# Kernel optimization log

Measured on AMD Instinct MI355X. Metric: run time of the kernel, lower is better.

The kernel has to match this reference:

```python
import jax, jax.numpy as jnp
import numpy as np

TOP_K = 3
K3, S3, P3 = 3, 1, 1  # unfold_kernel_size, stride, padding (lv3)


def unfold(x, k, stride, pad):
    """torch.nn.functional.unfold: [N,C,H,W] -> [N, C*k*k, L]."""
    patches = jax.lax.conv_general_dilated_patches(
        x, (k, k), (stride, stride), [(pad, pad), (pad, pad)],
        dimension_numbers=('NCHW', 'OIHW', 'NCHW'))  # [N, C*k*k, gh, gw]
    n, d, gh, gw = patches.shape
    return patches.reshape(n, d, gh * gw)


def fold(cols, H, W, k, stride, pad):
    """torch.nn.functional.fold (col2im, overlap-add): [N,C*k*k,L] -> [N,C,H,W]."""
    n, d, L = cols.shape
    C = d // (k * k)
    gh = (H + 2 * pad - k) // stride + 1
    gw = (W + 2 * pad - k) // stride + 1
    cols = cols.reshape(n, C, k, k, gh, gw)
    out = jnp.zeros((n, C, H + 2 * pad, W + 2 * pad), cols.dtype)
    for i in range(k):
        for j in range(k):
            out = out.at[:, :, i:i + stride * gh:stride,
                         j:j + stride * gw:stride].add(cols[:, :, i, j])
    return out[:, :, pad:pad + H, pad:pad + W]


def _l2norm(x, axis):
    # F.normalize: x / max(||x||_2, 1e-12)
    return x / jnp.maximum(jnp.sqrt(jnp.sum(x * x, axis=axis, keepdims=True)), 1e-12)


def search_transfer(lr_lv3, refsr_lv3, ref_lv1, ref_lv2, ref_lv3):
    n, _, h, w = lr_lv3.shape
    k2, s2, p2 = 2 * K3, 2 * S3, 2 * P3
    k1, s1, p1 = 4 * K3, 4 * S3, 4 * P3

    # --- SearchPatches (original passes padding=stride, stride=padding; equal here) ---
    Q = unfold(lr_lv3, K3, P3, S3)            # [N, D, Lq]
    Kc = unfold(refsr_lv3, K3, P3, S3)        # [N, D, Lr]
    Kn = _l2norm(jnp.swapaxes(Kc, 1, 2), 2)   # [N, Lr, D]
    Qn = _l2norm(Q, 1)                        # [N, D, Lq]
    R = jnp.einsum('nrd,ndq->nrq', Kn, Qn)    # cosine sims [N, Lr, Lq]
    vals, idx = jax.lax.top_k(jnp.swapaxes(R, 1, 2), TOP_K)  # [N, Lq, K]
    soft = jnp.swapaxes(vals, 1, 2)           # [N, K, Lq]
    hard = jnp.swapaxes(idx, 1, 2)            # [N, K, Lq]

    # --- Transfer: unfold ref textures (padding=stride per original code) ---
    V3 = unfold(ref_lv3, K3, S3, S3)          # [N, 256*9,  Lq]
    V2 = unfold(ref_lv2, k2, s2, s2)          # [N, 128*36, Lq]
    V1 = unfold(ref_lv1, k1, s1, s1)          # [N, 64*144, Lq]

    # overlap divisors are constant across top-k iterations -> compute once
    div3 = fold(jnp.ones_like(V3), h, w, K3, S3, S3)
    div2 = fold(jnp.ones_like(V2), 2 * h, 2 * w, k2, s2, s2)
    div1 = fold(jnp.ones_like(V1), 4 * h, 4 * w, k1, s1, s1)

    Sl, T3l, T2l, T1l = [], [], [], []
    for i in range(TOP_K):
        hi = hard[:, i, :][:, None, :]        # [N, 1, Lq], broadcasts over feature dim
        g3 = jnp.take_along_axis(V3, hi, axis=2)
        g2 = jnp.take_along_axis(V2, hi, axis=2)
        g1 = jnp.take_along_axis(V1, hi, axis=2)
        T3l.append(fold(g3, h, w, K3, S3, S3) / div3)
        T2l.append(fold(g2, 2 * h, 2 * w, k2, s2, s2) / div2)
        T1l.append(fold(g1, 4 * h, 4 * w, k1, s1, s1) / div1)
        Sl.append(soft[:, i, :].reshape(n, 1, h // S3, w // S3))
    return (jnp.stack(Sl), jnp.stack(T3l), jnp.stack(T2l), jnp.stack(T1l))


def setup_inputs() -> dict:
    key = jax.random.key(0)
    ks = jax.random.split(key, 5)
    return {
        'lr_lv3':    jax.random.normal(ks[0], (2, 256, 48, 48),   dtype=jnp.float32),
        'refsr_lv3': jax.random.normal(ks[1], (2, 256, 48, 48),   dtype=jnp.float32),
        'ref_lv1':   jax.random.normal(ks[2], (2, 64, 192, 192),  dtype=jnp.float32),
        'ref_lv2':   jax.random.normal(ks[3], (2, 128, 96, 96),   dtype=jnp.float32),
        'ref_lv3':   jax.random.normal(ks[4], (2, 256, 48, 48),   dtype=jnp.float32),
    }


def reference(lr_lv3, refsr_lv3, ref_lv1, ref_lv2, ref_lv3):
    return search_transfer(lr_lv3, refsr_lv3, ref_lv1, ref_lv2, ref_lv3)
```

## Files before the change

### kernel.cpp

```cpp
#include <hip/hip_runtime.h>
#include <cfloat>
#include <cstdint>
#include <cstddef>

#define N_B 2
#define C3v 256
#define Gg 48
#define Lq 2304
#define NCHUNK 64
#define CHUNK 36

typedef __attribute__((ext_vector_type(8))) short short8;
typedef __attribute__((ext_vector_type(4))) float f32x4;
typedef unsigned short u16;

__device__ inline float bf2f(u16 h) {
    return __builtin_bit_cast(float, (unsigned)h << 16);
}
__device__ inline u16 f2bf_rne(float v) {
    unsigned u = __builtin_bit_cast(unsigned, v);
    unsigned r = (u + 0x7FFFu + ((u >> 16) & 1u)) >> 16;
    return (u16)r;
}


__global__ void sqnorm_kernel(const float* __restrict__ refsr, const float* __restrict__ lr,
                              float* __restrict__ sref, float* __restrict__ sq) {
    int which = blockIdx.z, n = blockIdx.y;
    int p = blockIdx.x * 256 + threadIdx.x;
    const float* src = (which ? lr : refsr) + (size_t)n * C3v * Lq + p;
    float s = 0.f;
#pragma unroll 8
    for (int c = 0; c < C3v; ++c) { float v = src[(size_t)c * Lq]; s = fmaf(v, v, s); }
    (which ? sq : sref)[n * Lq + p] = s;
}

__global__ void invnorm_kernel(const float* __restrict__ sref, const float* __restrict__ sq,
                               float* __restrict__ invK, float* __restrict__ invQ) {
    int which = blockIdx.z, n = blockIdx.y;
    int p = blockIdx.x * 256 + threadIdx.x;
    int py = p / Gg, px = p - (p / Gg) * Gg;
    const float* S = (which ? sq : sref) + n * Lq;
    float s = 0.f;
    for (int oy = -1; oy <= 1; ++oy) {
        int y = py + oy; if ((unsigned)y >= Gg) continue;
        for (int ox = -1; ox <= 1; ++ox) {
            int x = px + ox; if ((unsigned)x >= Gg) continue;
            s += S[y * Gg + x];
        }
    }
    (which ? invQ : invK)[n * Lq + p] = 1.0f / fmaxf(sqrtf(s), 1e-12f);
}

__global__ void conv_split(const float* __restrict__ X, const float* __restrict__ Y,
                           u16* __restrict__ XH, u16* __restrict__ XL,
                           u16* __restrict__ YH, u16* __restrict__ YL) {
    __shared__ float tsm[16][17];
    int z = blockIdx.z; int which = z & 1, n = z >> 1;
    const float* src = (which ? Y : X) + (size_t)n * C3v * Lq;
    u16* H = (which ? YH : XH) + (size_t)n * Lq * C3v;
    u16* L = (which ? YL : XL) + (size_t)n * Lq * C3v;
    int p0 = blockIdx.x * 16, c0 = blockIdx.y * 16;
    int tx = threadIdx.x & 15, ty = threadIdx.x >> 4;
    tsm[ty][tx] = src[(size_t)(c0 + ty) * Lq + p0 + tx];
    __syncthreads();
    float v = tsm[tx][ty];
    u16 h = f2bf_rne(v);
    float hv = bf2f(h);
    u16 l = f2bf_rne(v - hv);
    size_t o = (size_t)(p0 + ty) * C3v + c0 + tx;
    H[o] = h; L[o] = l;
}

__global__ __launch_bounds__(256) void gemm_mfma(const u16* __restrict__ XH_, const u16* __restrict__ XL_,
                                                 const u16* __restrict__ YH_, const u16* __restrict__ YL_,
                                                 float* __restrict__ C0) {
    int n = blockIdx.z;
    int r0 = blockIdx.y * 128, q0 = blockIdx.x * 128;
    const u16* XH = XH_ + (size_t)n * Lq * C3v;
    const u16* XL = XL_ + (size_t)n * Lq * C3v;
    const u16* YH = YH_ + (size_t)n * Lq * C3v;
    const u16* YL = YL_ + (size_t)n * Lq * C3v;
    float* Cb = C0 + (size_t)n * Lq * Lq;
    __shared__ __align__(16) u16 lds[16384];
    u16* AH = lds; u16* AL = lds + 4096; u16* BH = lds + 8192; u16* BL = lds + 12288;
    int t = threadIdx.x;
    int srow = t >> 1, sh = t & 1;
    const u16* gXH = XH + (size_t)(r0 + srow) * C3v + sh * 16;
    const u16* gXL = XL + (size_t)(r0 + srow) * C3v + sh * 16;
    const u16* gYH = YH + (size_t)(q0 + srow) * C3v + sh * 16;
    const u16* gYL = YL + (size_t)(q0 + srow) * C3v + sh * 16;
    int sidx = (sh * 2) * 1024 + srow * 8;
    int lane = t & 63, w = t >> 6;
    int wr = (w >> 1) * 64, wq = (w & 1) * 64;
    int fr = lane & 15, kg = lane >> 4;
    int ridx = kg * 1024 + fr * 8;
    f32x4 acc[4][4];
#pragma unroll
    for (int i = 0; i < 4; ++i)
#pragma unroll
        for (int j = 0; j < 4; ++j) acc[i][j] = (f32x4){0.f, 0.f, 0.f, 0.f};

    uint4 pXH0 = *(const uint4*)(gXH), pXH1 = *(const uint4*)(gXH + 8);
    uint4 pXL0 = *(const uint4*)(gXL), pXL1 = *(const uint4*)(gXL + 8);
    uint4 pYH0 = *(const uint4*)(gYH), pYH1 = *(const uint4*)(gYH + 8);
    uint4 pYL0 = *(const uint4*)(gYL), pYL1 = *(const uint4*)(gYL + 8);

    for (int c0 = 0; c0 < C3v; c0 += 32) {
        __syncthreads();
        *(uint4*)&AH[sidx] = pXH0; *(uint4*)&AH[sidx + 1024] = pXH1;
        *(uint4*)&AL[sidx] = pXL0; *(uint4*)&AL[sidx + 1024] = pXL1;
        *(uint4*)&BH[sidx] = pYH0; *(uint4*)&BH[sidx + 1024] = pYH1;
        *(uint4*)&BL[sidx] = pYL0; *(uint4*)&BL[sidx + 1024] = pYL1;
        __syncthreads();
        if (c0 + 32 < C3v) {
            pXH0 = *(const uint4*)(gXH + c0 + 32); pXH1 = *(const uint4*)(gXH + c0 + 40);
            pXL0 = *(const uint4*)(gXL + c0 + 32); pXL1 = *(const uint4*)(gXL + c0 + 40);
            pYH0 = *(const uint4*)(gYH + c0 + 32); pYH1 = *(const uint4*)(gYH + c0 + 40);
            pYL0 = *(const uint4*)(gYL + c0 + 32); pYL1 = *(const uint4*)(gYL + c0 + 40);
        }
        short8 ah[4], al[4];
#pragma unroll
        for (int fi = 0; fi < 4; ++fi) {
            ah[fi] = *(const short8*)&AH[ridx + (wr + fi * 16) * 8];
            al[fi] = *(const short8*)&AL[ridx + (wr + fi * 16) * 8];
        }
#pragma unroll
        for (int fj = 0; fj < 4; ++fj) {
            short8 bh = *(const short8*)&BH[ridx + (wq + fj * 16) * 8];
            short8 bl = *(const short8*)&BL[ridx + (wq + fj * 16) * 8];
#pragma unroll
            for (int fi = 0; fi < 4; ++fi) {
                acc[fi][fj] = __builtin_amdgcn_mfma_f32_16x16x32_bf16(al[fi], bh, acc[fi][fj], 0, 0, 0);
                acc[fi][fj] = __builtin_amdgcn_mfma_f32_16x16x32_bf16(ah[fi], bl, acc[fi][fj], 0, 0, 0);
                acc[fi][fj] = __builtin_amdgcn_mfma_f32_16x16x32_bf16(ah[fi], bh, acc[fi][fj], 0, 0, 0);
            }
        }
    }
    int orow = (lane >> 4) * 4;
#pragma unroll
    for (int fi = 0; fi < 4; ++fi)
#pragma unroll
        for (int fj = 0; fj < 4; ++fj)
#pragma unroll
            for (int j = 0; j < 4; ++j)
                Cb[(size_t)(r0 + wr + fi * 16 + orow + j) * Lq + q0 + wq + fj * 16 + fr] = acc[fi][fj][j];
}

__global__ __launch_bounds__(256) void topk_stage1(const float* __restrict__ C0, const float* __restrict__ invK,
                                                   float* __restrict__ ptv, int* __restrict__ pti) {
    int n = blockIdx.z;
    int ck = blockIdx.y;
    int q = blockIdx.x * 256 + threadIdx.x;
    int qy = q / Gg, qx = q - (q / Gg) * Gg;
    bool qvy0 = qy >= 1, qvy2 = qy <= Gg - 2;
    bool qvx0 = qx >= 1, qvx2 = qx <= Gg - 2;
    const float* Cb = C0 + (size_t)n * Lq * Lq + q;
    const float* iK = invK + n * Lq;
    float t0 = -FLT_MAX, t1 = -FLT_MAX, t2 = -FLT_MAX;
    int i0 = -1, i1 = -1, i2 = -1;
    int r_end = ck * CHUNK + CHUNK;
#pragma unroll 2
    for (int r = ck * CHUNK; r < r_end; ++r) {
        int ry = r / Gg, rx = r - (r / Gg) * Gg;
        const float* base = Cb + (size_t)r * Lq;
        float raw = 0.f;
#pragma unroll
        for (int oy = -1; oy <= 1; ++oy) {
            bool my = ((unsigned)(ry + oy) < Gg) && (oy < 0 ? qvy0 : (oy > 0 ? qvy2 : true));
#pragma unroll
            for (int ox = -1; ox <= 1; ++ox) {
                bool m = my && ((unsigned)(rx + ox) < Gg) && (ox < 0 ? qvx0 : (ox > 0 ? qvx2 : true));
                ptrdiff_t o = (ptrdiff_t)(oy * Gg + ox) * (Lq + 1);
                float ld = base[o];
                raw += m ? ld : 0.f;
            }
        }
        float v = raw * iK[r];
        if (v > t0)      { t2 = t1; i2 = i1; t1 = t0; i1 = i0; t0 = v; i0 = r; }
        else if (v > t1) { t2 = t1; i2 = i1; t1 = v;  i1 = r; }
        else if (v > t2) { t2 = v;  i2 = r; }
    }
    size_t off = ((size_t)(n * NCHUNK + ck) * Lq + q) * 3;
    ptv[off] = t0; ptv[off + 1] = t1; ptv[off + 2] = t2;
    pti[off] = i0; pti[off + 1] = i1; pti[off + 2] = i2;
}

__global__ void topk_stage2(const float* __restrict__ ptv, const int* __restrict__ pti,
                            const float* __restrict__ invQ, int* __restrict__ hard,
                            float* __restrict__ Sout) {
    int g = blockIdx.x * 256 + threadIdx.x;
    if (g >= N_B * Lq) return;
    int n = g / Lq, q = g - n * Lq;
    float t0 = -FLT_MAX, t1 = -FLT_MAX, t2 = -FLT_MAX;
    int i0 = -1, i1 = -1, i2 = -1;
    for (int ck = 0; ck < NCHUNK; ++ck) {
        size_t off = ((size_t)(n * NCHUNK + ck) * Lq + q) * 3;
#pragma unroll
        for (int j = 0; j < 3; ++j) {
            float v = ptv[off + j]; int idx = pti[off + j];
            if (v > t0)      { t2 = t1; i2 = i1; t1 = t0; i1 = i0; t0 = v; i0 = idx; }
            else if (v > t1) { t2 = t1; i2 = i1; t1 = v;  i1 = idx; }
            else if (v > t2) { t2 = v;  i2 = idx; }
        }
    }
    float iq = invQ[g];
    Sout[0 * (N_B * Lq) + g] = t0 * iq;
    Sout[1 * (N_B * Lq) + g] = t1 * iq;
    Sout[2 * (N_B * Lq) + g] = t2 * iq;
    hard[(n * 3 + 0) * Lq + q] = i0;
    hard[(n * 3 + 1) * Lq + q] = i1;
    hard[(n * 3 + 2) * Lq + q] = i2;
}

__global__ void nchw_to_nhwc_bf16(const float* __restrict__ in, u16* __restrict__ out,
                                  int C, int H, int W) {
    __shared__ float t[16][17];
    int bz = blockIdx.z; int n = bz / H; int y = bz - n * H;
    int x0 = blockIdx.x * 16, c0 = blockIdx.y * 16;
    int tx = threadIdx.x & 15, ty = threadIdx.x >> 4;
    t[ty][tx] = in[(((size_t)n * C + c0 + ty) * H + y) * W + x0 + tx];
    __syncthreads();
    out[(((size_t)n * H + y) * W + x0 + ty) * C + c0 + tx] = f2bf_rne(t[tx][ty]);
}


__global__ __launch_bounds__(256) void t3_kernel(const int* __restrict__ hard, const u16* __restrict__ img_,
                                                 float* __restrict__ out) {
    int i = blockIdx.z >> 1, n = blockIdx.z & 1;
    int u = blockIdx.y;
    int w0 = blockIdx.x * 4;
    int c = threadIdx.x;
    const int* hb = hard + (size_t)(n * 3 + i) * Lq;
    const u16* img = img_ + (size_t)n * Lq * C3v;
    int cyc = 3 - (u == 0) - (u == Gg - 1);
    int rxA[3][6], spA[3][6];
    bool svA[3][6];
#pragma unroll
    for (int oa = 0; oa < 3; ++oa) {
        int gy = u - (oa - 1);
        bool gyv = (unsigned)gy < Gg;
#pragma unroll
        for (int x = 0; x < 6; ++x) {
            int gx = w0 - 1 + x;
            bool gv = gyv & ((unsigned)gx < Gg);
            int r = hb[(gv ? gy : 0) * Gg + (gv ? gx : 0)];
            int ry = r / Gg, rx = r - (r / Gg) * Gg;
            int syb = ry + (oa - 1);
            bool sval = gv & ((unsigned)syb < Gg);
            rxA[oa][x] = rx;
            spA[oa][x] = (sval ? syb : 0) * Gg;
            svA[oa][x] = sval;
        }
    }
    float rr[4];
#pragma unroll
    for (int k = 0; k < 4; ++k) {
        int w = w0 + k;
        int cxc = 3 - (w == 0) - (w == Gg - 1);
        float acc = 0.f;
#pragma unroll
        for (int oa = 0; oa < 3; ++oa)
#pragma unroll
            for (int ob = 0; ob < 3; ++ob) {
                int x = k + 2 - ob;
                int sxb = rxA[oa][x] + (ob - 1);
                bool sv = svA[oa][x] & ((unsigned)sxb < Gg);
                float ld = bf2f(img[((size_t)(spA[oa][x] + (sv ? sxb : 0))) * C3v + c]);
                acc += sv ? ld : 0.f;
            }
        rr[k] = acc / (float)(cyc * cxc);
    }
    float4 vv = make_float4(rr[0], rr[1], rr[2], rr[3]);
    *(float4*)&out[(((size_t)(i * N_B + n) * C3v + c) * Lq) + u * Gg + w0] = vv;
}

__global__ __launch_bounds__(256) void t2_kernel(const int* __restrict__ hard, const u16* __restrict__ img_,
                                                 float* __restrict__ out) {
    const int C = 128, Him = 96;
    int i = blockIdx.z >> 1, n = blockIdx.z & 1;
    int u = blockIdx.y;
    int w0 = blockIdx.x * 4;
    int c = threadIdx.x & 127, v = threadIdx.x >> 7;
    const int* hb = hard + (size_t)(n * 3 + i) * Lq;
    const u16* img = img_ + (size_t)n * Him * Him * C;
    int cyc = 3 - (u == 0) - (u == Gg - 1);
    int rxA[3][6], syA[3][6];
    bool svA[3][6];
#pragma unroll
    for (int oa = 0; oa < 3; ++oa) {
        int gy = u - (oa - 1);
        bool gyv = (unsigned)gy < Gg;
#pragma unroll
        for (int x = 0; x < 6; ++x) {
            int gx = w0 - 1 + x;
            bool gv = gyv & ((unsigned)gx < Gg);
            int r = hb[(gv ? gy : 0) * Gg + (gv ? gx : 0)];
            int ry = r / Gg, rx = r - (r / Gg) * Gg;
            int syb = ry + (oa - 1);
            bool sval = gv & ((unsigned)syb < Gg);
            rxA[oa][x] = rx;
            syA[oa][x] = 2 * (sval ? syb : 0) + v;
            svA[oa][x] = sval;
        }
    }
#pragma unroll
    for (int k = 0; k < 4; ++k) {
        int w = w0 + k;
        int cxc = 3 - (w == 0) - (w == Gg - 1);
        float a0 = 0.f, a1 = 0.f;
#pragma unroll
        for (int oa = 0; oa < 3; ++oa)
#pragma unroll
            for (int ob = 0; ob < 3; ++ob) {
                int x = k + 2 - ob;
                int sxb = rxA[oa][x] + (ob - 1);
                bool sv = svA[oa][x] & ((unsigned)sxb < Gg);
                int sxc = sv ? sxb : 0;
                const u16* row = &img[((size_t)syA[oa][x] * Him + 2 * sxc) * C + c];
                float l0 = bf2f(row[0]), l1 = bf2f(row[C]);
                a0 += sv ? l0 : 0.f;
                a1 += sv ? l1 : 0.f;
            }
        float d = (float)(cyc * cxc);
        *(float2*)&out[(((size_t)(i * N_B + n) * C + c) * (Him * Him)) + (2 * u + v) * Him + 2 * w] =
            make_float2(a0 / d, a1 / d);
    }
}

template <bool NHWC>
__global__ __launch_bounds__(256) void t1_kernel(const int* __restrict__ hard, const void* __restrict__ img_,
                                                 float* __restrict__ out) {
    const int C = 64, Him = 192;
    int i = blockIdx.z >> 1, n = blockIdx.z & 1;
    int u = blockIdx.y;
    int w0 = blockIdx.x * 4;
    int c = threadIdx.x & 63, v = threadIdx.x >> 6;
    const int* hb = hard + (size_t)(n * 3 + i) * Lq;
    const u16* img = (const u16*)img_ + (size_t)n * Him * Him * C;
    const float* imgf = (const float*)img_;
    int cyc = 3 - (u == 0) - (u == Gg - 1);
    int rxA[3][6], syA[3][6];
    bool svA[3][6];
#pragma unroll
    for (int oa = 0; oa < 3; ++oa) {
        int gy = u - (oa - 1);
        bool gyv = (unsigned)gy < Gg;
#pragma unroll
        for (int x = 0; x < 6; ++x) {
            int gx = w0 - 1 + x;
            bool gv = gyv & ((unsigned)gx < Gg);
            int r = hb[(gv ? gy : 0) * Gg + (gv ? gx : 0)];
            int ry = r / Gg, rx = r - (r / Gg) * Gg;
            int syb = ry + (oa - 1);
            bool sval = gv & ((unsigned)syb < Gg);
            rxA[oa][x] = rx;
            syA[oa][x] = 4 * (sval ? syb : 0) + v;
            svA[oa][x] = sval;
        }
    }
    float4 res[4];
#pragma unroll
    for (int k = 0; k < 4; ++k) {
        int w = w0 + k;
        int cxc = 3 - (w == 0) - (w == Gg - 1);
        float z0 = 0.f, z1 = 0.f, z2 = 0.f, z3 = 0.f;
#pragma unroll
        for (int oa = 0; oa < 3; ++oa)
#pragma unroll
            for (int ob = 0; ob < 3; ++ob) {
                int x = k + 2 - ob;
                int sxb = rxA[oa][x] + (ob - 1);
                bool sv = svA[oa][x] & ((unsigned)sxb < Gg);
                int sxc = sv ? sxb : 0;
                int sy = syA[oa][x], sx = 4 * sxc;
                float l0, l1, l2, l3;
                if (NHWC) {
                    const u16* row = &img[((size_t)sy * Him + sx) * C + c];
                    l0 = bf2f(row[0]); l1 = bf2f(row[C]); l2 = bf2f(row[2 * C]); l3 = bf2f(row[3 * C]);
                } else {
                    const float* row = &imgf[(((size_t)(n * C + c)) * Him + sy) * Him + sx];
                    l0 = row[0]; l1 = row[1]; l2 = row[2]; l3 = row[3];
                }
                z0 += sv ? l0 : 0.f;
                z1 += sv ? l1 : 0.f;
                z2 += sv ? l2 : 0.f;
                z3 += sv ? l3 : 0.f;
            }
        float d = (float)(cyc * cxc);
        res[k] = make_float4(z0 / d, z1 / d, z2 / d, z3 / d);
    }
    size_t ob_ = (((size_t)(i * N_B + n) * C + c) * (Him * Him)) + (4 * u + v) * Him + 4 * w0;
#pragma unroll
    for (int k = 0; k < 4; ++k) *(float4*)&out[ob_ + 4 * k] = res[k];
}


extern "C" void kernel_launch(void* const* d_in, const int* in_sizes, int n_in,
                              void* d_out, int out_size, void* d_ws, size_t ws_size,
                              hipStream_t stream) {
    (void)in_sizes; (void)n_in; (void)out_size;
    const float* lr    = (const float*)d_in[0];
    const float* refsr = (const float*)d_in[1];
    const float* ref1  = (const float*)d_in[2];
    const float* ref2  = (const float*)d_in[3];
    const float* ref3  = (const float*)d_in[4];
    float* out = (float*)d_out;

    const size_t S_OFF  = 0;
    const size_t T3_OFF = 13824;
    const size_t T2_OFF = 3552768;
    const size_t T1_OFF = 10630656;

    float* wsf  = (float*)d_ws;
    float* sref = wsf;
    float* sq   = wsf + 4608;
    float* invK = wsf + 2 * 4608;
    float* invQ = wsf + 3 * 4608;
    int*   hard = (int*)(wsf + 4 * 4608);
    size_t small_elems = 4 * 4608 + 13824;
    size_t small_bytes = small_elems * 4;

    float* ptv = out + T3_OFF;
    int*   pti = (int*)(ptv + (size_t)N_B * NCHUNK * Lq * 3);

    u16* XHp = (u16*)(out + T2_OFF);
    u16* XLp = XHp + (size_t)N_B * Lq * C3v;
    u16* YHp = XLp + (size_t)N_B * Lq * C3v;
    u16* YLp = YHp + (size_t)N_B * Lq * C3v;

    const size_t GUARD = 120000;
    size_t big_off  = (small_bytes + 255) & ~(size_t)255;
    size_t big_need = (2 * (size_t)Lq * Lq + 2 * GUARD) * 4;
    bool primary = (ws_size >= big_off + big_need);
    float* big = primary ? (float*)((char*)d_ws + big_off) : (out + T1_OFF);
    float* C0    = big + GUARD;
    u16* nhwc3 = (u16*)big;
    u16* nhwc2 = nhwc3 + (size_t)N_B * Lq * C3v;
    u16* nhwc1 = nhwc2 + (size_t)N_B * 96 * 96 * 128;

    sqnorm_kernel <<<dim3(9, 2, 2),  256, 0, stream>>>(refsr, lr, sref, sq);
    invnorm_kernel<<<dim3(9, 2, 2),  256, 0, stream>>>(sref, sq, invK, invQ);
    conv_split    <<<dim3(144, 16, 4), 256, 0, stream>>>(refsr, lr, XHp, XLp, YHp, YLp);
    gemm_mfma     <<<dim3(18, 18, 2), 256, 0, stream>>>(XHp, XLp, YHp, YLp, C0);
    topk_stage1   <<<dim3(9, NCHUNK, 2), 256, 0, stream>>>(C0, invK, ptv, pti);
    topk_stage2   <<<dim3(18), 256, 0, stream>>>(ptv, pti, invQ, hard, out + S_OFF);
    nchw_to_nhwc_bf16<<<dim3(3, 16, 2 * 48),  256, 0, stream>>>(ref3, nhwc3, 256, 48, 48);
    nchw_to_nhwc_bf16<<<dim3(6, 8,  2 * 96),  256, 0, stream>>>(ref2, nhwc2, 128, 96, 96);
    if (primary)
        nchw_to_nhwc_bf16<<<dim3(12, 4, 2 * 192), 256, 0, stream>>>(ref1, nhwc1, 64, 192, 192);
    t3_kernel<<<dim3(12, 48, 6), 256, 0, stream>>>(hard, nhwc3, out + T3_OFF);
    t2_kernel<<<dim3(12, 48, 6), 256, 0, stream>>>(hard, nhwc2, out + T2_OFF);
    if (primary) t1_kernel<true> <<<dim3(12, 48, 6), 256, 0, stream>>>(hard, nhwc1, out + T1_OFF);
    else         t1_kernel<false><<<dim3(12, 48, 6), 256, 0, stream>>>(hard, ref1, out + T1_OFF);
}
```

Measured before the change: 238.4 us.

## Split 3x3 correlation stencil into separable x pass then y pass in top-k

Replaces the 9-tap diagonal stencil over the correlation matrix inside topk_stage1 with a separable two-pass approach: a vectorized stencil_x kernel that sums the horizontal neighbours into a temporary buffer, then a top-k kernel that reads only three vertical taps. This cuts per-element loads in the top-k scan but adds a full extra write and read of the Lq x Lq matrix. It also multi-accumulates the sqnorm reduction and parallelizes topk_stage2 across four chunk groups with a shared-memory merge. The temp buffer is placed in the T1 output region with a guard offset, which relies on that region being unused at this point.

```diff
diff --git a/kernel.cpp b/kernel.cpp
--- a/kernel.cpp
+++ b/kernel.cpp
@@ -9,6 +9,9 @@
 #define Lq 2304
 #define NCHUNK 64
 #define CHUNK 36
+#define OXS 2305
+#define OYS 110640
+#define TGUARD 110848
 
 typedef __attribute__((ext_vector_type(8))) short short8;
 typedef __attribute__((ext_vector_type(4))) float f32x4;
@@ -29,10 +32,17 @@
     int which = blockIdx.z, n = blockIdx.y;
     int p = blockIdx.x * 256 + threadIdx.x;
     const float* src = (which ? lr : refsr) + (size_t)n * C3v * Lq + p;
-    float s = 0.f;
-#pragma unroll 8
-    for (int c = 0; c < C3v; ++c) { float v = src[(size_t)c * Lq]; s = fmaf(v, v, s); }
-    (which ? sq : sref)[n * Lq + p] = s;
+    float s0 = 0.f, s1 = 0.f, s2 = 0.f, s3 = 0.f;
+#pragma unroll 4
+    for (int c = 0; c < C3v; c += 4) {
+        float v0 = src[(size_t)c * Lq];
+        float v1 = src[(size_t)(c + 1) * Lq];
+        float v2 = src[(size_t)(c + 2) * Lq];
+        float v3 = src[(size_t)(c + 3) * Lq];
+        s0 = fmaf(v0, v0, s0); s1 = fmaf(v1, v1, s1);
+        s2 = fmaf(v2, v2, s2); s3 = fmaf(v3, v3, s3);
+    }
+    (which ? sq : sref)[n * Lq + p] = (s0 + s1) + (s2 + s3);
 }
 
 __global__ void invnorm_kernel(const float* __restrict__ sref, const float* __restrict__ sq,
@@ -147,8 +157,69 @@
                 Cb[(size_t)(r0 + wr + fi * 16 + orow + j) * Lq + q0 + wq + fj * 16 + fr] = acc[fi][fj][j];
 }
 
-__global__ __launch_bounds__(256) void topk_stage1(const float* __restrict__ C0, const float* __restrict__ invK,
-                                                   float* __restrict__ ptv, int* __restrict__ pti) {
+__global__ __launch_bounds__(256) void stencil_x(const float* __restrict__ C0, float* __restrict__ Tm) {
+    size_t idx = ((size_t)blockIdx.x * 256 + threadIdx.x) * 4;
+    int col = (int)(idx % Lq);
+    int rowg = (int)(idx / Lq);
+    int r = rowg - (rowg >= Lq ? Lq : 0);
+    int rx = r % Gg;
+    int qx = col % Gg;
+    bool rL = rx >= 1, rR = rx <= Gg - 2;
+    float4 la = *(const float4*)&C0[idx - 2308];
+    float4 lb = *(const float4*)&C0[idx - 2304];
+    float4 cc = *(const float4*)&C0[idx];
+    float4 ra = *(const float4*)&C0[idx + 2304];
+    float4 rb = *(const float4*)&C0[idx + 2308];
+    float lv[4] = {la.w, lb.x, lb.y, lb.z};
+    float cv[4] = {cc.x, cc.y, cc.z, cc.w};
+    float rv[4] = {ra.y, ra.z, ra.w, rb.x};
+    float ov[4];
+#pragma unroll
+    for (int e = 0; e < 4; ++e) {
+        bool mL = rL & ((qx + e) >= 1);
+        bool mR = rR & ((qx + e) <= Gg - 2);
+        float v = (mL ? lv[e] : 0.f) + cv[e];
+        v += (mR ? rv[e] : 0.f);
+        ov[e] = v;
+    }
+    *(float4*)&Tm[idx] = make_float4(ov[0], ov[1], ov[2], ov[3]);
+}
+
+__global__ __launch_bounds__(256) void topk_stage1_sep(const float* __restrict__ Tm, const float* __restrict__ invK,
+                                                       float* __restrict__ ptv, int* __restrict__ pti) {
+    int n = blockIdx.z;
+    int ck = blockIdx.y;
+    int q = blockIdx.x * 256 + threadIdx.x;
+    int qy = q / Gg;
+    bool qvy0 = qy >= 1, qvy2 = qy <= Gg - 2;
+    const float* Tb = Tm + (size_t)n * Lq * Lq + q;
+    const float* iK = invK + n * Lq;
+    float t0 = -FLT_MAX, t1 = -FLT_MAX, t2 = -FLT_MAX;
+    int i0 = -1, i1 = -1, i2 = -1;
+    int r_end = ck * CHUNK + CHUNK;
+#pragma unroll 4
+    for (int r = ck * CHUNK; r < r_end; ++r) {
+        int ry = r / Gg;
+        size_t p = (size_t)r * Lq;
+        float top = Tb[p - OYS];
+        float mid = Tb[p];
+        float bot = Tb[p + OYS];
+        bool mT = (ry >= 1) & qvy0;
+        bool mB = (ry <= Gg - 2) & qvy2;
+        float raw = (mT ? top : 0.f) + mid;
+        raw += (mB ? bot : 0.f);
+        float v = raw * iK[r];
+        if (v > t0)      { t2 = t1; i2 = i1; t1 = t0; i1 = i0; t0 = v; i0 = r; }
+        else if (v > t1) { t2 = t1; i2 = i1; t1 = v;  i1 = r; }
+        else if (v > t2) { t2 = v;  i2 = r; }
+    }
+    size_t off = ((size_t)(n * NCHUNK + ck) * Lq + q) * 3;
+    ptv[off] = t0; ptv[off + 1] = t1; ptv[off + 2] = t2;
+    pti[off] = i0; pti[off + 1] = i1; pti[off + 2] = i2;
+}
+
+__global__ __launch_bounds__(256) void topk_stage1_direct(const float* __restrict__ C0, const float* __restrict__ invK,
+                                                          float* __restrict__ ptv, int* __restrict__ pti) {
     int n = blockIdx.z;
     int ck = blockIdx.y;
     int q = blockIdx.x * 256 + threadIdx.x;
@@ -186,31 +257,49 @@
     pti[off] = i0; pti[off + 1] = i1; pti[off + 2] = i2;
 }
 
-__global__ void topk_stage2(const float* __restrict__ ptv, const int* __restrict__ pti,
-                            const float* __restrict__ invQ, int* __restrict__ hard,
-                            float* __restrict__ Sout) {
-    int g = blockIdx.x * 256 + threadIdx.x;
-    if (g >= N_B * Lq) return;
+__global__ __launch_bounds__(256) void topk_stage2(const float* __restrict__ ptv, const int* __restrict__ pti,
+                                                   const float* __restrict__ invQ, int* __restrict__ hard,
+                                                   float* __restrict__ Sout) {
+    __shared__ float sv[64][4][3];
+    __shared__ int   si[64][4][3];
+    int ql = threadIdx.x & 63, j = threadIdx.x >> 6;
+    int g = blockIdx.x * 64 + ql;
     int n = g / Lq, q = g - n * Lq;
     float t0 = -FLT_MAX, t1 = -FLT_MAX, t2 = -FLT_MAX;
     int i0 = -1, i1 = -1, i2 = -1;
-    for (int ck = 0; ck < NCHUNK; ++ck) {
+    int ck0 = j * (NCHUNK / 4);
+    for (int ck = ck0; ck < ck0 + NCHUNK / 4; ++ck) {
         size_t off = ((size_t)(n * NCHUNK + ck) * Lq + q) * 3;
 #pragma unroll
-        for (int j = 0; j < 3; ++j) {
-            float v = ptv[off + j]; int idx = pti[off + j];
+        for (int m = 0; m < 3; ++m) {
+            float v = ptv[off + m]; int idx = pti[off + m];
             if (v > t0)      { t2 = t1; i2 = i1; t1 = t0; i1 = i0; t0 = v; i0 = idx; }
             else if (v > t1) { t2 = t1; i2 = i1; t1 = v;  i1 = idx; }
             else if (v > t2) { t2 = v;  i2 = idx; }
         }
     }
-    float iq = invQ[g];
-    Sout[0 * (N_B * Lq) + g] = t0 * iq;
-    Sout[1 * (N_B * Lq) + g] = t1 * iq;
-    Sout[2 * (N_B * Lq) + g] = t2 * iq;
-    hard[(n * 3 + 0) * Lq + q] = i0;
-    hard[(n * 3 + 1) * Lq + q] = i1;
-    hard[(n * 3 + 2) * Lq + q] = i2;
+    sv[ql][j][0] = t0; sv[ql][j][1] = t1; sv[ql][j][2] = t2;
+    si[ql][j][0] = i0; si[ql][j][1] = i1; si[ql][j][2] = i2;
+    __syncthreads();
+    if (j == 0) {
+        t0 = t1 = t2 = -FLT_MAX; i0 = i1 = i2 = -1;
+#pragma unroll
+        for (int jj = 0; jj < 4; ++jj)
+#pragma unroll
+            for (int m = 0; m < 3; ++m) {
+                float v = sv[ql][jj][m]; int idx = si[ql][jj][m];
+                if (v > t0)      { t2 = t1; i2 = i1; t1 = t0; i1 = i0; t0 = v; i0 = idx; }
+                else if (v > t1) { t2 = t1; i2 = i1; t1 = v;  i1 = idx; }
+                else if (v > t2) { t2 = v;  i2 = idx; }
+            }
+        float iq = invQ[g];
+        Sout[0 * (N_B * Lq) + g] = t0 * iq;
+        Sout[1 * (N_B * Lq) + g] = t1 * iq;
+        Sout[2 * (N_B * Lq) + g] = t2 * iq;
+        hard[(n * 3 + 0) * Lq + q] = i0;
+        hard[(n * 3 + 1) * Lq + q] = i1;
+        hard[(n * 3 + 2) * Lq + q] = i2;
+    }
 }
 
 __global__ void nchw_to_nhwc_bf16(const float* __restrict__ in, u16* __restrict__ out,
@@ -429,6 +518,8 @@
     u16* YHp = XLp + (size_t)N_B * Lq * C3v;
     u16* YLp = YHp + (size_t)N_B * Lq * C3v;
 
+    float* Tm = out + T1_OFF + TGUARD;
+
     const size_t GUARD = 120000;
     size_t big_off  = (small_bytes + 255) & ~(size_t)255;
     size_t big_need = (2 * (size_t)Lq * Lq + 2 * GUARD) * 4;
@@ -443,8 +534,13 @@
     invnorm_kernel<<<dim3(9, 2, 2),  256, 0, stream>>>(sref, sq, invK, invQ);
     conv_split    <<<dim3(144, 16, 4), 256, 0, stream>>>(refsr, lr, XHp, XLp, YHp, YLp);
     gemm_mfma     <<<dim3(18, 18, 2), 256, 0, stream>>>(XHp, XLp, YHp, YLp, C0);
-    topk_stage1   <<<dim3(9, NCHUNK, 2), 256, 0, stream>>>(C0, invK, ptv, pti);
-    topk_stage2   <<<dim3(18), 256, 0, stream>>>(ptv, pti, invQ, hard, out + S_OFF);
+    if (primary) {
+        stencil_x       <<<dim3(10368), 256, 0, stream>>>(C0, Tm);
+        topk_stage1_sep <<<dim3(9, NCHUNK, 2), 256, 0, stream>>>(Tm, invK, ptv, pti);
+    } else {
+        topk_stage1_direct<<<dim3(9, NCHUNK, 2), 256, 0, stream>>>(C0, invK, ptv, pti);
+    }
+    topk_stage2   <<<dim3(72), 256, 0, stream>>>(ptv, pti, invQ, hard, out + S_OFF);
     nchw_to_nhwc_bf16<<<dim3(3, 16, 2 * 48),  256, 0, stream>>>(ref3, nhwc3, 256, 48, 48);
     nchw_to_nhwc_bf16<<<dim3(6, 8,  2 * 96),  256, 0, stream>>>(ref2, nhwc2, 128, 96, 96);
     if (primary)
```

New measurement: 234.5 us. Within noise of the previous version (-1.6%).
